# Kernel optimization log

Hardware: AMD Instinct MI355X
Metric: run time of the kernel (lower is better)

Reference implementation:

```python
import jax, jax.numpy as jnp
import numpy as np

B, C, H, W = 2, 64, 64, 128
HW = H * W
PCR = (0.0, -25.6, -3.0, 51.2, 25.6, 1.0)  # point cloud range x/y/z min, x/y/z max
VOX = (0.1, 0.1, 4.0)                      # voxel size
NX = int(round((PCR[3] - PCR[0]) / VOX[0]))  # 512
NY = int(round((PCR[4] - PCR[1]) / VOX[1]))  # 512
BIG = 1e10  # masked-out distance (avoid inf for clean vjp)


def _rand_points(key):
    k_xyz, k_i = jax.random.split(key)
    u = jax.random.uniform(k_xyz, (B, 3, H, W), jnp.float32)
    lo = jnp.array([PCR[0], PCR[1], PCR[2]], jnp.float32).reshape(1, 3, 1, 1)
    hi = jnp.array([PCR[3], PCR[4], PCR[5]], jnp.float32).reshape(1, 3, 1, 1)
    xyz = lo + u * (hi - lo)
    inten = jax.random.uniform(k_i, (B, 1, H, W), jnp.float32)
    return jnp.concatenate([xyz, inten], axis=1)  # (B,4,H,W)


def setup_inputs() -> dict:
    key = jax.random.key(0)
    k1, k2, k3, k4, k5 = jax.random.split(key, 5)
    return {
        "fv_features": jax.random.normal(k1, (B, C, H, W), jnp.float32),
        "points_img": _rand_points(k2),
        "proj_masks": jax.random.randint(k4, (B, H, W), 0, 2).astype(jnp.int32),
        "points_img_far": _rand_points(k3),
        "proj_masks_far": jax.random.randint(k5, (B, H, W), 0, 2).astype(jnp.int32),
    }


def _three_interpolate(near_pts, near_feats, near_valid, far_pts):
    """pointnet2 three_nn + three_interpolate with invalid near points masked.
    near_pts: (N,3), near_feats: (N,C), near_valid: (N,) bool, far_pts: (M,3).
    Returns interpolated far features (M,C)."""
    # squared distances via |a|^2 + |b|^2 - 2 a.b  -> (M, N), avoids (M,N,3) temp
    d2 = (jnp.sum(far_pts * far_pts, -1)[:, None]
          + jnp.sum(near_pts * near_pts, -1)[None, :]
          - 2.0 * far_pts @ near_pts.T)
    d2 = jnp.where(near_valid[None, :], d2, BIG)
    neg_d, idx = jax.lax.top_k(-d2, 3)        # 3 nearest near-points per far point
    dist = -neg_d                              # squared dists, as in pointnet2 CUDA
    dist_recip = 1.0 / (dist + 1e-8)
    weight = dist_recip / jnp.sum(dist_recip, axis=-1, keepdims=True)  # (M,3)
    gathered = near_feats[idx]                 # (M,3,C)
    return jnp.einsum('mk,mkc->mc', weight, gathered)


def _scatter_bev(pts, feats, valid):
    """Mean-scatter point features into the BEV grid. pts:(N,3) feats:(N,C) valid:(N,)."""
    ix = jnp.floor((pts[:, 0] - PCR[0]) / VOX[0]).astype(jnp.int32)
    iy = jnp.floor((pts[:, 1] - PCR[1]) / VOX[1]).astype(jnp.int32)
    in_range = (ix >= 0) & (ix < NX) & (iy >= 0) & (iy < NY)
    w = (valid & in_range).astype(feats.dtype)            # zero-weight invalid pts
    flat = jnp.clip(iy, 0, NY - 1) * NX + jnp.clip(ix, 0, NX - 1)
    sums = jnp.zeros((NY * NX, feats.shape[1]), feats.dtype).at[flat].add(feats * w[:, None])
    cnt = jnp.zeros((NY * NX,), feats.dtype).at[flat].add(w)
    bev = sums / jnp.maximum(cnt, 1.0)[:, None]
    return bev.reshape(NY, NX, -1).transpose(2, 0, 1)      # (C, NY, NX)


def reference(fv_features, points_img, proj_masks, points_img_far, proj_masks_far):
    feats = fv_features.transpose(0, 2, 3, 1).reshape(B, HW, C)
    pts = points_img[:, :3].transpose(0, 2, 3, 1).reshape(B, HW, 3)
    pts_far = points_img_far[:, :3].transpose(0, 2, 3, 1).reshape(B, HW, 3)
    m = proj_masks.reshape(B, HW) > 0
    m_far = proj_masks_far.reshape(B, HW) > 0
    outs = []
    for k in range(B):  # small fixed batch loop, mirrors original per-sample loop
        interp = _three_interpolate(pts[k], feats[k], m[k], pts_far[k])
        all_pts = jnp.concatenate([pts[k], pts_far[k]], axis=0)
        all_feats = jnp.concatenate([feats[k], interp], axis=0)
        all_valid = jnp.concatenate([m[k], m_far[k]], axis=0)
        outs.append(_scatter_bev(all_pts, all_feats, all_valid))
    return jnp.stack(outs, axis=0)  # (B, C, NY, NX)
```

## Files before the change

kernel.cpp:

```cpp
#include <hip/hip_runtime.h>
#include <math.h>

constexpr int B_  = 2;
constexpr int C_  = 64;
constexpr int HW_ = 64 * 128;
constexpr int N_  = HW_;
constexpr int NX_ = 512;
constexpr int NY_ = 512;
constexpr int NYNX_ = NX_ * NY_;
constexpr int GC_  = 32;
constexpr int GCC_ = GC_ * GC_;
constexpr int CAP_ = 48;
constexpr int LPF_ = 8;
constexpr int BN_  = B_ * N_;
constexpr int NNB_ = BN_ / (256 / LPF_);
constexpr int NSB_ = BN_ / 32;
constexpr int MAXSLOT_ = 32768;

__device__ __forceinline__ int voxel_of(float x, float y, float w) {
#pragma clang fp contract(off)
  if (w == 0.0f) return -1;
  float qx = (x - 0.0f) / 0.1f;
  float qy = (y - (-25.6f)) / 0.1f;
  int ix = (int)floorf(qx);
  int iy = (int)floorf(qy);
  if (ix < 0 || ix >= NX_ || iy < 0 || iy >= NY_) return -1;
  return iy * NX_ + ix;
}

__device__ __forceinline__ int gcell_x(float x) {
  int c = (int)floorf(x * 0.625f);
  return min(GC_ - 1, max(0, c));
}
__device__ __forceinline__ int gcell_y(float y) {
  int c = (int)floorf((y + 25.6f) * 0.625f);
  return min(GC_ - 1, max(0, c));
}

__device__ __forceinline__ int alloc_slot(int* nslot) {
  unsigned long long mk = __ballot(1);
  int lane = threadIdx.x & 63;
  int lead = __ffsll((unsigned long long)mk) - 1;
  int nact = __popcll(mk);
  int basep = 0;
  if (lane == lead) basep = atomicAdd(nslot, nact);
  basep = __shfl(basep, lead);
  return basep + __popcll(mk & ((1ull << lane) - 1ull));
}

__global__ __launch_bounds__(256) void prep_kernel(
    const float* __restrict__ fv,
    const float* __restrict__ pi, const int* __restrict__ pm,
    const float* __restrict__ pif, const int* __restrict__ pmf,
    float4* __restrict__ near4, float4* __restrict__ far4,
    float* __restrict__ cnt, int* __restrict__ gcellcnt,
    int* __restrict__ nslot, int* __restrict__ slotmap,
    float4* __restrict__ gpts, int* __restrict__ gidx,
    float* __restrict__ fvT) {
#pragma clang fp contract(off)
  __shared__ float tile[64][65];
  if (blockIdx.x < 64) {
    int t = blockIdx.x * 256 + threadIdx.x;
    int k = t / N_, n = t % N_;
    const float* base  = pi  + (size_t)k * 4 * HW_;
    const float* basef = pif + (size_t)k * 4 * HW_;
    float x = base[n], y = base[HW_ + n], z = base[2 * HW_ + n];
    bool v = pm[k * HW_ + n] > 0;
    near4[t] = make_float4(x, y, z, v ? 1.0f : 0.0f);
    float fx = basef[n], fy = basef[HW_ + n], fz = basef[2 * HW_ + n];
    bool vf = pmf[k * HW_ + n] > 0;
    far4[t] = make_float4(fx, fy, fz, vf ? 1.0f : 0.0f);

    if (v) {
      float sq = (x * x + y * y) + z * z;
      int c = gcell_y(y) * GC_ + gcell_x(x);
      int p = atomicAdd(&gcellcnt[k * GCC_ + c], 1);
      if (p < CAP_) {
        size_t o = (size_t)(k * GCC_ + c) * CAP_ + p;
        gpts[o] = make_float4(x, y, z, sq);
        gidx[o] = n;
      }
    }

    int vn = voxel_of(x, y, v ? 1.0f : 0.0f);
    if (vn >= 0) {
      int kv = k * NYNX_ + vn;
      float old = atomicAdd(&cnt[kv], 1.0f);
      if (old == 0.0f) slotmap[kv] = alloc_slot(nslot) + 1;
    }
    int vfv = voxel_of(fx, fy, vf ? 1.0f : 0.0f);
    if (vfv >= 0) {
      int kv = k * NYNX_ + vfv;
      float old2 = atomicAdd(&cnt[kv], 1.0f);
      if (old2 == 0.0f) slotmap[kv] = alloc_slot(nslot) + 1;
    }
  } else {
    int bid = blockIdx.x - 64;
    int k = bid >> 7;
    int n0 = (bid & 127) * 64;
    int tx = threadIdx.x & 63, ty = threadIdx.x >> 6;
    for (int c = ty; c < C_; c += 4)
      tile[c][tx] = fv[((size_t)(k * C_ + c)) * HW_ + n0 + tx];
    __syncthreads();
    for (int nn = ty; nn < 64; nn += 4)
      fvT[((size_t)(k * HW_ + n0 + nn)) * C_ + tx] = tile[tx][nn];
  }
}

__device__ __forceinline__ void merge3L(float tv, int idx,
                                        float& b0, float& b1, float& b2,
                                        int& i0, int& i1, int& i2) {
  bool w0 = (tv < b0) || (tv == b0 && idx < i0);
  bool w1 = (tv < b1) || (tv == b1 && idx < i1);
  bool w2 = (tv < b2) || (tv == b2 && idx < i2);
  float ob0 = b0, ob1 = b1;
  int   oi0 = i0, oi1 = i1;
  b0 = w0 ? tv : b0;                    i0 = w0 ? idx : i0;
  b1 = w0 ? ob0 : (w1 ? tv : b1);       i1 = w0 ? oi0 : (w1 ? idx : i1);
  b2 = w1 ? ob1 : (w2 ? tv : b2);       i2 = w1 ? oi1 : (w2 ? idx : i2);
}

__global__ __launch_bounds__(256) void nn_scatter_kernel(
    const float4* __restrict__ far4, const int* __restrict__ gcellcnt,
    const float4* __restrict__ gpts, const int* __restrict__ gidx,
    const float4* __restrict__ near4, const float* __restrict__ fvT,
    const float* __restrict__ cnt, const int* __restrict__ slotmap,
    float* __restrict__ acc) {
#pragma clang fp contract(off)
  int tid = threadIdx.x;
  if (blockIdx.x < (unsigned)NNB_) {
    int q = tid & (LPF_ - 1);
    int g = blockIdx.x * (256 / LPF_) + (tid / LPF_);
    int k = g >> 13;
    int m = g & (N_ - 1);

    float4 f = far4[k * N_ + m];
    if (f.w == 0.0f) return;

    float sf = (f.x * f.x + f.y * f.y) + f.z * f.z;
    float ax = 2.0f * f.x, ay = 2.0f * f.y, az = 2.0f * f.z;
    int fcx = gcell_x(f.x), fcy = gcell_y(f.y);
    const int* gcc_ = gcellcnt + k * GCC_;

    float b0 = 1e30f, b1 = 1e30f, b2 = 1e30f;
    int i0 = 0, i1 = 0, i2 = 0;

    for (int r = 0; r < GC_; ++r) {
      int nc = (r == 0) ? 1 : 8 * r;
      for (int i = q; i < nc; i += LPF_) {
        int dx, dy;
        if (r == 0)            { dx = 0;             dy = 0; }
        else if (i < 2*r + 1)  { dx = i - r;         dy = -r; }
        else if (i < 4*r + 2)  { dx = i - (3*r + 1); dy = r; }
        else if (i < 6*r + 1)  { dx = -r;            dy = i - (5*r + 1); }
        else                   { dx = r;             dy = i - 7*r; }
        int cx = fcx + dx, cy = fcy + dy;
        if (cx < 0 || cx >= GC_ || cy < 0 || cy >= GC_) continue;
        int c = cy * GC_ + cx;
        int e = gcc_[c];
        if (e > CAP_) e = CAP_;
        const float4* gp = gpts + (size_t)(k * GCC_ + c) * CAP_;
        const int*    gi = gidx + (size_t)(k * GCC_ + c) * CAP_;
        for (int j = 0; j < e; ++j) {
          float4 p = gp[j];
          int idx = gi[j];
          float p0 = ax * p.x;
          float mm = __builtin_fmaf(az, p.z, __builtin_fmaf(ay, p.y, p0));
          float tv = (sf + p.w) - mm;
          merge3L(tv, idx, b0, b1, b2, i0, i1, i2);
        }
      }
      float s2 = b2;
      s2 = fminf(s2, __shfl_xor(s2, 1));
      s2 = fminf(s2, __shfl_xor(s2, 2));
      s2 = fminf(s2, __shfl_xor(s2, 4));
      float rd = (float)r * 1.6f;
      if (rd * rd > s2 + 0.01f) break;
    }

    int base = tid & ~(LPF_ - 1);
    for (int s = 1; s < LPF_; ++s) {
      float v0 = __shfl(b0, base + s), v1 = __shfl(b1, base + s), v2 = __shfl(b2, base + s);
      int   j0 = __shfl(i0, base + s), j1 = __shfl(i1, base + s), j2 = __shfl(i2, base + s);
      if (q == 0) {
        merge3L(v0, j0, b0, b1, b2, i0, i1, i2);
        merge3L(v1, j1, b0, b1, b2, i0, i1, i2);
        merge3L(v2, j2, b0, b1, b2, i0, i1, i2);
      }
    }
    float w0_ = 0.0f, w1_ = 0.0f, w2_ = 0.0f;
    if (q == 0) {
      float r0 = 1.0f / (b0 + 1e-8f);
      float r1 = 1.0f / (b1 + 1e-8f);
      float r2 = 1.0f / (b2 + 1e-8f);
      float rs = (r0 + r1) + r2;
      w0_ = r0 / rs; w1_ = r1 / rs; w2_ = r2 / rs;
    }
    float w0 = __shfl(w0_, base), w1 = __shfl(w1_, base), w2 = __shfl(w2_, base);
    int   j0 = __shfl(i0, base),  j1 = __shfl(i1, base),  j2 = __shfl(i2, base);

    int v = voxel_of(f.x, f.y, f.w);
    if (v < 0) return;
    int kv = k * NYNX_ + v;
    float cn = cnt[kv];
    size_t rowoff = (size_t)(slotmap[kv] - 1) * C_;
    const float4* r0p = (const float4*)(fvT + ((size_t)(k * N_ + j0)) * C_);
    const float4* r1p = (const float4*)(fvT + ((size_t)(k * N_ + j1)) * C_);
    const float4* r2p = (const float4*)(fvT + ((size_t)(k * N_ + j2)) * C_);
#pragma unroll
    for (int h = 0; h < 2; ++h) {
      int c4 = q * 2 + h;
      float4 a = r0p[c4], b = r1p[c4], c = r2p[c4];
      float4 val;
      val.x = (w0 * a.x + w1 * b.x) + w2 * c.x;
      val.y = (w0 * a.y + w1 * b.y) + w2 * c.y;
      val.z = (w0 * a.z + w1 * b.z) + w2 * c.z;
      val.w = (w0 * a.w + w1 * b.w) + w2 * c.w;
      if (cn == 1.0f) {
        ((float4*)(acc + rowoff))[c4] = val;
      } else {
        float* p = acc + rowoff + c4 * 4;
        atomicAdd(p + 0, val.x); atomicAdd(p + 1, val.y);
        atomicAdd(p + 2, val.z); atomicAdd(p + 3, val.w);
      }
    }
  } else {
    int q = tid & 7;
    int g = (blockIdx.x - NNB_) * 32 + (tid >> 3);
    int k = g >> 13;
    int n = g & (N_ - 1);
    float4 pt = near4[k * N_ + n];
    if (pt.w == 0.0f) return;
    int v = voxel_of(pt.x, pt.y, pt.w);
    if (v < 0) return;
    int kv = k * NYNX_ + v;
    float cn = cnt[kv];
    size_t rowoff = (size_t)(slotmap[kv] - 1) * C_;
    const float4* src = (const float4*)(fvT + ((size_t)(k * N_ + n)) * C_);
#pragma unroll
    for (int h = 0; h < 2; ++h) {
      int c4 = q * 2 + h;
      float4 val = src[c4];
      if (cn == 1.0f) {
        ((float4*)(acc + rowoff))[c4] = val;
      } else {
        float* p = acc + rowoff + c4 * 4;
        atomicAdd(p + 0, val.x); atomicAdd(p + 1, val.y);
        atomicAdd(p + 2, val.z); atomicAdd(p + 3, val.w);
      }
    }
  }
}

__global__ __launch_bounds__(256) void emit_kernel(
    const float* __restrict__ acc, const float* __restrict__ cnt,
    const int* __restrict__ slotmap, float* __restrict__ out) {
#pragma clang fp contract(off)
  __shared__ float tile[64][65];
  __shared__ float cs[64];
  __shared__ int   sl[64];
  int t = threadIdx.x;
  int k = blockIdx.y;
  int v0 = blockIdx.x * 64;

  if (t < 64) {
    cs[t] = cnt[(size_t)k * NYNX_ + v0 + t];
    sl[t] = slotmap[(size_t)k * NYNX_ + v0 + t];
  }
  __syncthreads();

  const float4* acc4 = (const float4*)acc;
#pragma unroll
  for (int p = 0; p < 4; ++p) {
    int row = p * 16 + (t >> 4);
    int f4  = t & 15;
    float c = cs[row];
    float4 a = make_float4(0.0f, 0.0f, 0.0f, 0.0f);
    if (c > 0.0f) {
      a = acc4[(size_t)(sl[row] - 1) * (C_ / 4) + f4];
      a.x /= c; a.y /= c; a.z /= c; a.w /= c;
    }
    tile[f4 * 4 + 0][row] = a.x;
    tile[f4 * 4 + 1][row] = a.y;
    tile[f4 * 4 + 2][row] = a.z;
    tile[f4 * 4 + 3][row] = a.w;
  }
  __syncthreads();

#pragma unroll
  for (int p = 0; p < 4; ++p) {
    int c  = p * 16 + (t >> 4);
    int xq = t & 15;
    float4 o = make_float4(tile[c][xq * 4 + 0], tile[c][xq * 4 + 1],
                           tile[c][xq * 4 + 2], tile[c][xq * 4 + 3]);
    ((float4*)out)[(((size_t)k * C_ + c) * NYNX_ + v0) / 4 + xq] = o;
  }
}

extern "C" void kernel_launch(void* const* d_in, const int* in_sizes, int n_in,
                              void* d_out, int out_size, void* d_ws, size_t ws_size,
                              hipStream_t stream) {
  const float* fv  = (const float*)d_in[0];
  const float* pi  = (const float*)d_in[1];
  const int*   pm  = (const int*)d_in[2];
  const float* pif = (const float*)d_in[3];
  const int*   pmf = (const int*)d_in[4];
  float* out = (float*)d_out;

  char* wsb = (char*)d_ws;
  float*  fvT    = (float*)(wsb);
  float*  cnt    = (float*)(wsb + 4194304);
  int*    gcell  = (int*)(wsb + 6291456);
  int*    nslot  = (int*)(wsb + 6299648);
  int*    slotmap= (int*)(wsb + 6299664);
  float*  acc    = (float*)(wsb + 8396816);
  float4* near4  = (float4*)(wsb + 16785424);
  float4* far4   = (float4*)(wsb + 17047568);
  float4* gpts   = (float4*)(wsb + 17309712);
  int*    gidx   = (int*)(wsb + 18882576);

  hipMemsetAsync(cnt, 0, 12591120, stream);

  prep_kernel<<<320, 256, 0, stream>>>(
      fv, pi, pm, pif, pmf, near4, far4, cnt, gcell, nslot, slotmap,
      gpts, gidx, fvT);
  nn_scatter_kernel<<<NNB_ + NSB_, 256, 0, stream>>>(
      far4, gcell, gpts, gidx, near4, fvT, cnt, slotmap, acc);
  emit_kernel<<<dim3(NYNX_ / 64, B_), 256, 0, stream>>>(acc, cnt, slotmap, out);
}
```

Before: 185.6 us.

## Compact valid points into work lists and index accumulator directly by voxel

```diff
diff --git a/kernel.cpp b/kernel.cpp
--- a/kernel.cpp
+++ b/kernel.cpp
@@ -13,9 +13,8 @@
 constexpr int CAP_ = 48;
 constexpr int LPF_ = 8;
 constexpr int BN_  = B_ * N_;
-constexpr int NNB_ = BN_ / (256 / LPF_);
+constexpr int NNB_ = BN_ / 32;
 constexpr int NSB_ = BN_ / 32;
-constexpr int MAXSLOT_ = 32768;
 
 __device__ __forceinline__ int voxel_of(float x, float y, float w) {
 #pragma clang fp contract(off)
@@ -37,13 +36,12 @@
   return min(GC_ - 1, max(0, c));
 }
 
-__device__ __forceinline__ int alloc_slot(int* nslot) {
+__device__ __forceinline__ int wave_append(int* ctr) {
   unsigned long long mk = __ballot(1);
   int lane = threadIdx.x & 63;
   int lead = __ffsll((unsigned long long)mk) - 1;
-  int nact = __popcll(mk);
   int basep = 0;
-  if (lane == lead) basep = atomicAdd(nslot, nact);
+  if (lane == lead) basep = atomicAdd(ctr, __popcll(mk));
   basep = __shfl(basep, lead);
   return basep + __popcll(mk & ((1ull << lane) - 1ull));
 }
@@ -52,11 +50,11 @@
     const float* __restrict__ fv,
     const float* __restrict__ pi, const int* __restrict__ pm,
     const float* __restrict__ pif, const int* __restrict__ pmf,
-    float4* __restrict__ near4, float4* __restrict__ far4,
     float* __restrict__ cnt, int* __restrict__ gcellcnt,
-    int* __restrict__ nslot, int* __restrict__ slotmap,
+    int* __restrict__ nctr, float4* __restrict__ farlist,
+    int2* __restrict__ nearlist,
     float4* __restrict__ gpts, int* __restrict__ gidx,
-    float* __restrict__ fvT) {
+    float* __restrict__ acc, float* __restrict__ fvT) {
 #pragma clang fp contract(off)
   __shared__ float tile[64][65];
   if (blockIdx.x < 64) {
@@ -66,10 +64,8 @@
     const float* basef = pif + (size_t)k * 4 * HW_;
     float x = base[n], y = base[HW_ + n], z = base[2 * HW_ + n];
     bool v = pm[k * HW_ + n] > 0;
-    near4[t] = make_float4(x, y, z, v ? 1.0f : 0.0f);
     float fx = basef[n], fy = basef[HW_ + n], fz = basef[2 * HW_ + n];
     bool vf = pmf[k * HW_ + n] > 0;
-    far4[t] = make_float4(fx, fy, fz, vf ? 1.0f : 0.0f);
 
     if (v) {
       float sq = (x * x + y * y) + z * z;
@@ -82,17 +78,30 @@
       }
     }
 
+    float4 z4 = make_float4(0.0f, 0.0f, 0.0f, 0.0f);
     int vn = voxel_of(x, y, v ? 1.0f : 0.0f);
     if (vn >= 0) {
       int kv = k * NYNX_ + vn;
       float old = atomicAdd(&cnt[kv], 1.0f);
-      if (old == 0.0f) slotmap[kv] = alloc_slot(nslot) + 1;
+      if (old == 1.0f) {
+        float4* row = (float4*)(acc + (size_t)kv * C_);
+#pragma unroll
+        for (int i = 0; i < C_ / 4; ++i) row[i] = z4;
+      }
+      int p = wave_append(&nctr[1]);
+      nearlist[p] = make_int2(kv, t);
     }
     int vfv = voxel_of(fx, fy, vf ? 1.0f : 0.0f);
     if (vfv >= 0) {
       int kv = k * NYNX_ + vfv;
       float old2 = atomicAdd(&cnt[kv], 1.0f);
-      if (old2 == 0.0f) slotmap[kv] = alloc_slot(nslot) + 1;
+      if (old2 == 1.0f) {
+        float4* row = (float4*)(acc + (size_t)kv * C_);
+#pragma unroll
+        for (int i = 0; i < C_ / 4; ++i) row[i] = z4;
+      }
+      int p = wave_append(&nctr[0]);
+      farlist[p] = make_float4(fx, fy, fz, __int_as_float(kv));
     }
   } else {
     int bid = blockIdx.x - 64;
@@ -121,21 +130,22 @@
 }
 
 __global__ __launch_bounds__(256) void nn_scatter_kernel(
-    const float4* __restrict__ far4, const int* __restrict__ gcellcnt,
+    const int* __restrict__ nctr,
+    const float4* __restrict__ farlist, const int2* __restrict__ nearlist,
+    const int* __restrict__ gcellcnt,
     const float4* __restrict__ gpts, const int* __restrict__ gidx,
-    const float4* __restrict__ near4, const float* __restrict__ fvT,
-    const float* __restrict__ cnt, const int* __restrict__ slotmap,
-    float* __restrict__ acc) {
+    const float* __restrict__ fvT,
+    const float* __restrict__ cnt, float* __restrict__ acc) {
 #pragma clang fp contract(off)
   int tid = threadIdx.x;
   if (blockIdx.x < (unsigned)NNB_) {
     int q = tid & (LPF_ - 1);
     int g = blockIdx.x * (256 / LPF_) + (tid / LPF_);
-    int k = g >> 13;
-    int m = g & (N_ - 1);
-
-    float4 f = far4[k * N_ + m];
-    if (f.w == 0.0f) return;
+    if (g >= nctr[0]) return;
+
+    float4 f = farlist[g];
+    int kv = __float_as_int(f.w);
+    int k = kv >> 18;
 
     float sf = (f.x * f.x + f.y * f.y) + f.z * f.z;
     float ax = 2.0f * f.x, ay = 2.0f * f.y, az = 2.0f * f.z;
@@ -199,11 +209,8 @@
     float w0 = __shfl(w0_, base), w1 = __shfl(w1_, base), w2 = __shfl(w2_, base);
     int   j0 = __shfl(i0, base),  j1 = __shfl(i1, base),  j2 = __shfl(i2, base);
 
-    int v = voxel_of(f.x, f.y, f.w);
-    if (v < 0) return;
-    int kv = k * NYNX_ + v;
     float cn = cnt[kv];
-    size_t rowoff = (size_t)(slotmap[kv] - 1) * C_;
+    size_t rowoff = (size_t)kv * C_;
     const float4* r0p = (const float4*)(fvT + ((size_t)(k * N_ + j0)) * C_);
     const float4* r1p = (const float4*)(fvT + ((size_t)(k * N_ + j1)) * C_);
     const float4* r2p = (const float4*)(fvT + ((size_t)(k * N_ + j2)) * C_);
@@ -227,16 +234,12 @@
   } else {
     int q = tid & 7;
     int g = (blockIdx.x - NNB_) * 32 + (tid >> 3);
-    int k = g >> 13;
-    int n = g & (N_ - 1);
-    float4 pt = near4[k * N_ + n];
-    if (pt.w == 0.0f) return;
-    int v = voxel_of(pt.x, pt.y, pt.w);
-    if (v < 0) return;
-    int kv = k * NYNX_ + v;
+    if (g >= nctr[1]) return;
+    int2 e = nearlist[g];
+    int kv = e.x;
     float cn = cnt[kv];
-    size_t rowoff = (size_t)(slotmap[kv] - 1) * C_;
-    const float4* src = (const float4*)(fvT + ((size_t)(k * N_ + n)) * C_);
+    size_t rowoff = (size_t)kv * C_;
+    const float4* src = (const float4*)(fvT + (size_t)e.y * C_);
 #pragma unroll
     for (int h = 0; h < 2; ++h) {
       int c4 = q * 2 + h;
@@ -254,19 +257,15 @@
 
 __global__ __launch_bounds__(256) void emit_kernel(
     const float* __restrict__ acc, const float* __restrict__ cnt,
-    const int* __restrict__ slotmap, float* __restrict__ out) {
+    float* __restrict__ out) {
 #pragma clang fp contract(off)
   __shared__ float tile[64][65];
   __shared__ float cs[64];
-  __shared__ int   sl[64];
   int t = threadIdx.x;
   int k = blockIdx.y;
   int v0 = blockIdx.x * 64;
 
-  if (t < 64) {
-    cs[t] = cnt[(size_t)k * NYNX_ + v0 + t];
-    sl[t] = slotmap[(size_t)k * NYNX_ + v0 + t];
-  }
+  if (t < 64) cs[t] = cnt[(size_t)k * NYNX_ + v0 + t];
   __syncthreads();
 
   const float4* acc4 = (const float4*)acc;
@@ -277,7 +276,7 @@
     float c = cs[row];
     float4 a = make_float4(0.0f, 0.0f, 0.0f, 0.0f);
     if (c > 0.0f) {
-      a = acc4[(size_t)(sl[row] - 1) * (C_ / 4) + f4];
+      a = acc4[((size_t)k * NYNX_ + v0 + row) * (C_ / 4) + f4];
       a.x /= c; a.y /= c; a.z /= c; a.w /= c;
     }
     tile[f4 * 4 + 0][row] = a.x;
@@ -308,23 +307,22 @@
   float* out = (float*)d_out;
 
   char* wsb = (char*)d_ws;
-  float*  fvT    = (float*)(wsb);
-  float*  cnt    = (float*)(wsb + 4194304);
-  int*    gcell  = (int*)(wsb + 6291456);
-  int*    nslot  = (int*)(wsb + 6299648);
-  int*    slotmap= (int*)(wsb + 6299664);
-  float*  acc    = (float*)(wsb + 8396816);
-  float4* near4  = (float4*)(wsb + 16785424);
-  float4* far4   = (float4*)(wsb + 17047568);
-  float4* gpts   = (float4*)(wsb + 17309712);
-  int*    gidx   = (int*)(wsb + 18882576);
-
-  hipMemsetAsync(cnt, 0, 12591120, stream);
+  float*  fvT     = (float*)(wsb);
+  float*  cnt     = (float*)(wsb + 4194304);
+  int*    gcell   = (int*)(wsb + 6291456);
+  int*    nctr    = (int*)(wsb + 6299648);
+  float4* farlist = (float4*)(wsb + 6299664);
+  int2*   nearlist= (int2*)(wsb + 6561808);
+  float4* gpts    = (float4*)(wsb + 6692880);
+  int*    gidx    = (int*)(wsb + 8265744);
+  float*  acc     = (float*)(wsb + 16777216);
+
+  hipMemsetAsync(cnt, 0, 2105360, stream);
 
   prep_kernel<<<320, 256, 0, stream>>>(
-      fv, pi, pm, pif, pmf, near4, far4, cnt, gcell, nslot, slotmap,
-      gpts, gidx, fvT);
+      fv, pi, pm, pif, pmf, cnt, gcell, nctr, farlist, nearlist,
+      gpts, gidx, acc, fvT);
   nn_scatter_kernel<<<NNB_ + NSB_, 256, 0, stream>>>(
-      far4, gcell, gpts, gidx, near4, fvT, cnt, slotmap, acc);
-  emit_kernel<<<dim3(NYNX_ / 64, B_), 256, 0, stream>>>(acc, cnt, slotmap, out);
-}
+      nctr, farlist, nearlist, gcell, gpts, gidx, fvT, cnt, acc);
+  emit_kernel<<<dim3(NYNX_ / 64, B_), 256, 0, stream>>>(acc, cnt, out);
+}
```

Measured after the change: 182.8 us (median of 2 runs). Within noise of the previous version (-1.5%).
